# Optimization experiments

Measured on AMD Instinct MI355X. Metric: run time of the kernel, lower is better.

Reference implementation:

```python
import jax, jax.numpy as jnp
import numpy as np

D = 1024
KERNEL = 4

def setup_inputs() -> dict:
    key = jax.random.key(0)
    ks = jax.random.split(key, 8)
    B, L, d = 4, 8192, D
    x = jax.random.normal(ks[0], (B, L, d), dtype=jnp.float32)
    conv_weight = jax.random.normal(ks[1], (d, 1, KERNEL), dtype=jnp.float32) * 0.02
    conv_bias = jnp.zeros((d,), dtype=jnp.float32)
    lim = 1.0 / np.sqrt(d)
    Wr_w = jax.random.uniform(ks[2], (d, d), jnp.float32, -lim, lim)
    Wr_b = jax.random.uniform(ks[3], (d,), jnp.float32, -lim, lim)
    Wi_w = jax.random.uniform(ks[4], (d, d), jnp.float32, -lim, lim)
    Wi_b = jax.random.uniform(ks[5], (d,), jnp.float32, -lim, lim)
    log_a = jnp.full((d,), 7.5, dtype=jnp.float32)
    out_w = jax.random.uniform(ks[6], (d, d), jnp.float32, -lim, lim)
    norm_w = jnp.ones((d,), dtype=jnp.float32)
    return {"x": x, "conv_weight": conv_weight, "conv_bias": conv_bias,
            "Wr_w": Wr_w, "Wr_b": Wr_b, "Wi_w": Wi_w, "Wi_b": Wi_b,
            "log_a": log_a, "out_w": out_w, "norm_w": norm_w}

def _causal_depthwise_conv(x, w, b):
    # x: [B,L,d], w: [d,1,K], b: [d]. out[t] = sum_k w[:,0,k] * x[t-3+k] + b
    B, L, d = x.shape
    xp = jnp.pad(x, ((0, 0), (KERNEL - 1, 0), (0, 0)))
    out = b[None, None, :]
    for k in range(KERNEL):  # small fixed kernel loop
        out = out + xp[:, k:k + L, :] * w[:, 0, k][None, None, :]
    return out

def _parallel_scan(a_t, b_t):
    # h_t = a_t * h_{t-1} + b_t via log-space cumsum; float32 throughout
    a = a_t.astype(jnp.float32)
    b = b_t.astype(jnp.float32)
    log_A = jnp.clip(jnp.cumsum(jnp.log(jnp.clip(a, 1e-7)), axis=1), -80.0, None)
    A = jnp.exp(log_A)
    h = A * jnp.cumsum(b * jnp.exp(-log_A), axis=1)
    return h.astype(a_t.dtype)

def _rmsnorm(x, w, eps=1e-6):
    ms = jnp.mean(jnp.square(x.astype(jnp.float32)), axis=-1, keepdims=True)
    return (x * jax.lax.rsqrt(ms + eps)).astype(x.dtype) * w

def reference(x, conv_weight, conv_bias, Wr_w, Wr_b, Wi_w, Wi_b, log_a, out_w, norm_w):
    x_conv = _causal_depthwise_conv(x, conv_weight, conv_bias)          # [B,L,d]
    r_t = jax.nn.sigmoid(x_conv @ Wr_w.T + Wr_b)
    i_t = jax.nn.sigmoid(x_conv @ Wi_w.T + Wi_b)
    a_base = jax.nn.sigmoid(log_a.astype(jnp.float32)).astype(x.dtype)
    a_t = jnp.power(a_base[None, None, :], 8.0 * r_t)
    b_t = jnp.sqrt(jnp.clip(1.0 - a_t * a_t, 1e-6, None)) * (i_t * x_conv)
    h = _parallel_scan(a_t, b_t)
    return _rmsnorm(h @ out_w.T, norm_w)
```

## Files before the change

### kernel.cpp

```cpp
#include <hip/hip_runtime.h>
#include <hip/hip_bf16.h>

#define D 1024
#define KW 4
#define SEQL 8192
#define BATCH 4
#define MROWS (BATCH*SEQL)
#define SEG 32
#define NSEG (SEQL/SEG)

using bf16 = __hip_bfloat16;
typedef __attribute__((ext_vector_type(8))) short bf16x8_t;
typedef __attribute__((ext_vector_type(4))) float f32x4_t;

__device__ __forceinline__ float sigmoid_f(float x){ return 1.0f/(1.0f + __expf(-x)); }

__device__ __forceinline__ void gload_lds16(const bf16* g, bf16* l){
  __builtin_amdgcn_global_load_lds(
    (const __attribute__((address_space(1))) unsigned int*)g,
    (__attribute__((address_space(3))) unsigned int*)l,
    16, 0, 0);
}

__device__ __forceinline__ void bf16x2_unpack(unsigned int u, float& lo, float& hi){
  union { unsigned int i; float f; } a, b;
  a.i = (u & 0xffffu) << 16;
  b.i = u & 0xffff0000u;
  lo = a.f; hi = b.f;
}
__device__ __forceinline__ unsigned int bf16x2_pack(float lo, float hi){
  unsigned short l = __builtin_bit_cast(unsigned short, __float2bfloat16(lo));
  unsigned short h = __builtin_bit_cast(unsigned short, __float2bfloat16(hi));
  return (unsigned int)l | ((unsigned int)h << 16);
}

__global__ __launch_bounds__(256) void prep_k(const float* __restrict__ Wr, const float* __restrict__ Wi,
                                              const float* __restrict__ Wrb, const float* __restrict__ Wib,
                                              const float* __restrict__ Wo,
                                              bf16* __restrict__ W1, bf16* __restrict__ Wob,
                                              float* __restrict__ b1){
  int idx = blockIdx.x*256 + threadIdx.x;
  if (idx < 2*D*D){
    int n = idx >> 10;
    float v = (n < D) ? Wr[idx] : Wi[idx - D*D];
    W1[idx] = __float2bfloat16(v);
  } else if (idx < 3*D*D){
    int j = idx - 2*D*D;
    Wob[j] = __float2bfloat16(Wo[j]);
  }
  if (idx < 2*D){
    b1[idx] = (idx < D) ? Wrb[idx] : Wib[idx - D];
  }
}

__global__ __launch_bounds__(256) void conv_k(const float* __restrict__ x, const float* __restrict__ w,
                                              const float* __restrict__ bias,
                                              unsigned int* __restrict__ xcb){
  int idx = blockIdx.x*256 + threadIdx.x;
  int c4 = idx & 255;
  int c  = c4 * 4;
  int m  = idx >> 8;
  int l  = m & (SEQL-1);
  const float* wp = w + c*KW;
  f32x4_t t0 = *(const f32x4_t*)(wp);
  f32x4_t t1 = *(const f32x4_t*)(wp + 4);
  f32x4_t t2 = *(const f32x4_t*)(wp + 8);
  f32x4_t t3 = *(const f32x4_t*)(wp + 12);
  f32x4_t bb = *(const f32x4_t*)(bias + c);
  const float* xm = x + (size_t)m*D + c;
  f32x4_t v3 = *(const f32x4_t*)xm;
  f32x4_t z  = (f32x4_t){0.f,0.f,0.f,0.f};
  f32x4_t v2 = (l>=1)? *(const f32x4_t*)(xm - D)   : z;
  f32x4_t v1 = (l>=2)? *(const f32x4_t*)(xm - 2*D) : z;
  f32x4_t v0 = (l>=3)? *(const f32x4_t*)(xm - 3*D) : z;
  float a0 = bb[0] + t0[0]*v0[0] + t0[1]*v1[0] + t0[2]*v2[0] + t0[3]*v3[0];
  float a1 = bb[1] + t1[0]*v0[1] + t1[1]*v1[1] + t1[2]*v2[1] + t1[3]*v3[1];
  float a2 = bb[2] + t2[0]*v0[2] + t2[1]*v1[2] + t2[2]*v2[2] + t2[3]*v3[2];
  float a3 = bb[3] + t3[0]*v0[3] + t3[1]*v1[3] + t3[2]*v2[3] + t3[3]*v3[3];
  uint2 o;
  o.x = bf16x2_pack(a0, a1);
  o.y = bf16x2_pack(a2, a3);
  *(uint2*)(xcb + (size_t)m*512 + 2*c4) = o;
}

template<typename OutT> __device__ __forceinline__ void store_cvt(OutT* p, float v);
template<> __device__ __forceinline__ void store_cvt<float>(float* p, float v){ *p = v; }
template<> __device__ __forceinline__ void store_cvt<bf16>(bf16* p, float v){ *p = __float2bfloat16(v); }

#define MFMA_BF16(a,b,c) __builtin_amdgcn_mfma_f32_16x16x32_bf16((a),(b),(c),0,0,0)

#define GPHASE(buf, q, STAGE_STMT, WAIT_STMT) do{                         \
    bf16x8_t a0 = rdA(buf, 2*(q),   0);                                   \
    bf16x8_t a1 = rdA(buf, 2*(q),   1);                                   \
    bf16x8_t a2 = rdA(buf, 2*(q)+1, 0);                                   \
    bf16x8_t a3 = rdA(buf, 2*(q)+1, 1);                                   \
    if ((q) == 0){                                                        \
      b00 = rdB(buf,0,0); b01 = rdB(buf,0,1);                             \
      b10 = rdB(buf,1,0); b11 = rdB(buf,1,1);                             \
      b20 = rdB(buf,2,0); b21 = rdB(buf,2,1);                             \
      b30 = rdB(buf,3,0); b31 = rdB(buf,3,1);                             \
    }                                                                     \
    STAGE_STMT;                                                           \
    WAIT_STMT;                                                            \
    __builtin_amdgcn_s_barrier();                                         \
    asm volatile("s_waitcnt lgkmcnt(0)" ::: "memory");                    \
    __builtin_amdgcn_s_setprio(1);                                        \
    acc[2*(q)  ][0] = MFMA_BF16(a0, b00, acc[2*(q)  ][0]);                \
    acc[2*(q)  ][0] = MFMA_BF16(a1, b01, acc[2*(q)  ][0]);                \
    acc[2*(q)  ][1] = MFMA_BF16(a0, b10, acc[2*(q)  ][1]);                \
    acc[2*(q)  ][1] = MFMA_BF16(a1, b11, acc[2*(q)  ][1]);                \
    acc[2*(q)  ][2] = MFMA_BF16(a0, b20, acc[2*(q)  ][2]);                \
    acc[2*(q)  ][2] = MFMA_BF16(a1, b21, acc[2*(q)  ][2]);                \
    acc[2*(q)  ][3] = MFMA_BF16(a0, b30, acc[2*(q)  ][3]);                \
    acc[2*(q)  ][3] = MFMA_BF16(a1, b31, acc[2*(q)  ][3]);                \
    acc[2*(q)+1][0] = MFMA_BF16(a2, b00, acc[2*(q)+1][0]);                \
    acc[2*(q)+1][0] = MFMA_BF16(a3, b01, acc[2*(q)+1][0]);                \
    acc[2*(q)+1][1] = MFMA_BF16(a2, b10, acc[2*(q)+1][1]);                \
    acc[2*(q)+1][1] = MFMA_BF16(a3, b11, acc[2*(q)+1][1]);                \
    acc[2*(q)+1][2] = MFMA_BF16(a2, b20, acc[2*(q)+1][2]);                \
    acc[2*(q)+1][2] = MFMA_BF16(a3, b21, acc[2*(q)+1][2]);                \
    acc[2*(q)+1][3] = MFMA_BF16(a2, b30, acc[2*(q)+1][3]);                \
    acc[2*(q)+1][3] = MFMA_BF16(a3, b31, acc[2*(q)+1][3]);                \
    __builtin_amdgcn_s_setprio(0);                                        \
    __builtin_amdgcn_s_barrier();                                         \
}while(0)

#define WAIT_STEADY do{ if (it + 1 < nIter) asm volatile("s_waitcnt vmcnt(4)" ::: "memory"); \
                        else                asm volatile("s_waitcnt vmcnt(0)" ::: "memory"); }while(0)

template<typename OutT, bool HB>
__global__ __launch_bounds__(512, 2) void gemm256(const bf16* __restrict__ A, const bf16* __restrict__ B,
                                                  const float* __restrict__ bias, OutT* __restrict__ C,
                                                  int M, int N, int K){
  __shared__ alignas(128) bf16 Asm[2][256*64];
  __shared__ alignas(128) bf16 Bsm[2][256*64];
  const int t    = threadIdx.x;
  const int wave = t >> 6, lane = t & 63;
  const int wm   = wave >> 2, wn = wave & 3;
  const int lrow = lane & 15, quad = lane >> 4;

  const int nbn = N >> 8;
  const int cpx = gridDim.x >> 3;
  const int bid = blockIdx.x;
  const int swz = (bid & 7) * cpx + (bid >> 3);
  const int m0  = (swz / nbn) << 8;
  const int n0  = (swz % nbn) << 8;

  const int srow = wave*8 + (lane >> 3);
  const int scol = (((lane & 7) ^ (srow & 7)) << 3);

  auto stageA = [&](int tile, int half, int buf){
    const bf16* g = A + (size_t)(m0 + half*128 + srow)*K + tile*64 + scol;
    bf16* l = &Asm[buf][half*128*64 + wave*8*64];
    gload_lds16(g, l);
    gload_lds16(g + (size_t)64*K, l + 64*64);
  };
  auto stageB = [&](int tile, int half, int buf){
    const bf16* g = B + (size_t)(n0 + half*128 + srow)*K + tile*64 + scol;
    bf16* l = &Bsm[buf][half*128*64 + wave*8*64];
    gload_lds16(g, l);
    gload_lds16(g + (size_t)64*K, l + 64*64);
  };
  auto rdA = [&](int buf, int fi, int ks)->bf16x8_t{
    return *(const bf16x8_t*)&Asm[buf][(wm*128 + fi*16 + lrow)*64 + ((((ks)*4 + quad) ^ (lrow & 7)) << 3)];
  };
  auto rdB = [&](int buf, int j, int ks)->bf16x8_t{
    return *(const bf16x8_t*)&Bsm[buf][(wn*64 + j*16 + lrow)*64 + ((((ks)*4 + quad) ^ (lrow & 7)) << 3)];
  };

  f32x4_t acc[8][4];
  #pragma unroll
  for (int i=0;i<8;i++)
    #pragma unroll
    for (int j=0;j<4;j++) acc[i][j] = (f32x4_t){0.f,0.f,0.f,0.f};
  bf16x8_t b00,b01,b10,b11,b20,b21,b30,b31;

  const int nt    = K >> 6;
  const int nIter = nt >> 1;

  stageB(0, 0, 0); stageB(0, 1, 0);
  stageA(0, 0, 0); stageA(0, 1, 0);
  stageB(1, 0, 1); stageB(1, 1, 1);
  asm volatile("s_waitcnt vmcnt(4)" ::: "memory");
  __builtin_amdgcn_s_barrier();

  for (int it = 0; it < nIter; ++it){
    const int t1 = 2*it + 1, t2 = 2*it + 2, t3 = 2*it + 3;
    const bool ok2 = (t2 < nt), ok3 = (t3 < nt);
    GPHASE(0, 0, stageA(t1, 0, 1), );
    GPHASE(0, 1, stageA(t1, 1, 1), );
    GPHASE(0, 2, if (ok2) stageB(t2, 0, 0), );
    GPHASE(0, 3, if (ok2) stageB(t2, 1, 0), WAIT_STEADY);
    GPHASE(1, 0, if (ok2) stageA(t2, 0, 0), );
    GPHASE(1, 1, if (ok2) stageA(t2, 1, 0), );
    GPHASE(1, 2, if (ok3) stageB(t3, 0, 1), );
    GPHASE(1, 3, if (ok3) stageB(t3, 1, 1), WAIT_STEADY);
  }

  #pragma unroll
  for (int i=0;i<8;i++){
    #pragma unroll
    for (int j=0;j<4;j++){
      int gm0 = m0 + wm*128 + i*16 + quad*4;
      int gn  = n0 + wn*64  + j*16 + lrow;
      float bv = HB ? bias[gn] : 0.f;
      #pragma unroll
      for (int r=0;r<4;r++){
        store_cvt(&C[(size_t)(gm0 + r)*N + gn], acc[i][j][r] + bv);
      }
    }
  }
}

__global__ __launch_bounds__(256) void scan1_k(const unsigned int* __restrict__ ri,
                                               const unsigned int* __restrict__ xcb,
                                               const float* __restrict__ log_a,
                                               float* __restrict__ Aprod, float* __restrict__ Hend){
  int idx = blockIdx.x*256 + threadIdx.x;
  int c4 = idx & 255;
  int c  = c4*4;
  int bs = idx >> 8;
  int s  = bs & (NSEG-1);
  int b  = bs >> 8;
  size_t m0 = (size_t)b*SEQL + (size_t)s*SEG;
  f32x4_t la = *(const f32x4_t*)(log_a + c);
  float c1[4];
  #pragma unroll
  for (int j=0;j<4;j++) c1[j] = -8.f * log1pf(__expf(-la[j]));
  float A[4] = {1.f,1.f,1.f,1.f};
  float h[4] = {0.f,0.f,0.f,0.f};
  #pragma unroll 4
  for (int l=0; l<SEG; l++){
    size_t m = m0 + l;
    uint2 uzr = *(const uint2*)(ri  + m*1024 + 2*c4);
    uint2 uzi = *(const uint2*)(ri  + m*1024 + 512 + 2*c4);
    uint2 uxv = *(const uint2*)(xcb + m*512  + 2*c4);
    float zr[4], zi[4], xv[4];
    bf16x2_unpack(uzr.x, zr[0], zr[1]); bf16x2_unpack(uzr.y, zr[2], zr[3]);
    bf16x2_unpack(uzi.x, zi[0], zi[1]); bf16x2_unpack(uzi.y, zi[2], zi[3]);
    bf16x2_unpack(uxv.x, xv[0], xv[1]); bf16x2_unpack(uxv.y, xv[2], xv[3]);
    #pragma unroll
    for (int j=0;j<4;j++){
      float a  = __expf(c1[j] * sigmoid_f(zr[j]));
      float bt = sqrtf(fmaxf(1.f - a*a, 1e-6f)) * sigmoid_f(zi[j]) * xv[j];
      A[j] *= a;
      h[j]  = fmaf(a, h[j], bt);
    }
  }
  *(f32x4_t*)(Aprod + 4*(size_t)idx) = (f32x4_t){A[0],A[1],A[2],A[3]};
  *(f32x4_t*)(Hend  + 4*(size_t)idx) = (f32x4_t){h[0],h[1],h[2],h[3]};
}

__global__ __launch_bounds__(256) void scan2_k(const float* __restrict__ Aprod, const float* __restrict__ Hend,
                                               float* __restrict__ carry){
  int idx = blockIdx.x*256 + threadIdx.x;
  int c = idx & (D-1);
  int b = idx >> 10;
  float h = 0.f;
  #pragma unroll 8
  for (int s=0; s<NSEG; s++){
    int j = ((b*NSEG + s) << 10) + c;
    float a = Aprod[j];
    float e = Hend[j];
    carry[j] = h;
    h = fmaf(a, h, e);
  }
}

__global__ __launch_bounds__(256) void scan3_k(const unsigned int* __restrict__ ri,
                                               unsigned int* xcb,
                                               const float* __restrict__ log_a, const float* __restrict__ carry){
  int idx = blockIdx.x*256 + threadIdx.x;
  int c4 = idx & 255;
  int c  = c4*4;
  int bs = idx >> 8;
  int s  = bs & (NSEG-1);
  int b  = bs >> 8;
  size_t m0 = (size_t)b*SEQL + (size_t)s*SEG;
  f32x4_t la = *(const f32x4_t*)(log_a + c);
  float c1[4];
  #pragma unroll
  for (int j=0;j<4;j++) c1[j] = -8.f * log1pf(__expf(-la[j]));
  f32x4_t h4 = *(const f32x4_t*)(carry + 4*(size_t)idx);
  float h[4] = {h4[0], h4[1], h4[2], h4[3]};
  #pragma unroll 4
  for (int l=0; l<SEG; l++){
    size_t m = m0 + l;
    uint2 uzr = *(const uint2*)(ri  + m*1024 + 2*c4);
    uint2 uzi = *(const uint2*)(ri  + m*1024 + 512 + 2*c4);
    uint2 uxv = *(const uint2*)(xcb + m*512  + 2*c4);
    float zr[4], zi[4], xv[4];
    bf16x2_unpack(uzr.x, zr[0], zr[1]); bf16x2_unpack(uzr.y, zr[2], zr[3]);
    bf16x2_unpack(uzi.x, zi[0], zi[1]); bf16x2_unpack(uzi.y, zi[2], zi[3]);
    bf16x2_unpack(uxv.x, xv[0], xv[1]); bf16x2_unpack(uxv.y, xv[2], xv[3]);
    #pragma unroll
    for (int j=0;j<4;j++){
      float a  = __expf(c1[j] * sigmoid_f(zr[j]));
      float bt = sqrtf(fmaxf(1.f - a*a, 1e-6f)) * sigmoid_f(zi[j]) * xv[j];
      h[j] = fmaf(a, h[j], bt);
    }
    uint2 o;
    o.x = bf16x2_pack(h[0], h[1]);
    o.y = bf16x2_pack(h[2], h[3]);
    *(uint2*)(xcb + m*512 + 2*c4) = o;
  }
}

__global__ __launch_bounds__(256) void rms_k(float* __restrict__ y, const float* __restrict__ nw){
  int row = blockIdx.x;
  int t   = threadIdx.x;
  float* yr = y + (size_t)row*D;
  f32x4_t v = *(const f32x4_t*)(yr + t*4);
  float ss = v[0]*v[0] + v[1]*v[1] + v[2]*v[2] + v[3]*v[3];
  #pragma unroll
  for (int off=32; off>0; off>>=1) ss += __shfl_down(ss, off);
  __shared__ float red[4];
  if ((t & 63) == 0) red[t>>6] = ss;
  __syncthreads();
  float tot = red[0] + red[1] + red[2] + red[3];
  float scale = rsqrtf(tot * (1.f/D) + 1e-6f);
  f32x4_t w = *(const f32x4_t*)(nw + t*4);
  f32x4_t o;
  #pragma unroll
  for (int k=0;k<4;k++) o[k] = v[k]*scale*w[k];
  *(f32x4_t*)(yr + t*4) = o;
}

extern "C" void kernel_launch(void* const* d_in, const int* in_sizes, int n_in,
                              void* d_out, int out_size, void* d_ws, size_t ws_size,
                              hipStream_t stream) {
  const float* x     = (const float*)d_in[0];
  const float* convw = (const float*)d_in[1];
  const float* convb = (const float*)d_in[2];
  const float* Wr_w  = (const float*)d_in[3];
  const float* Wr_b  = (const float*)d_in[4];
  const float* Wi_w  = (const float*)d_in[5];
  const float* Wi_b  = (const float*)d_in[6];
  const float* log_a = (const float*)d_in[7];
  const float* out_w = (const float*)d_in[8];
  const float* norm_w= (const float*)d_in[9];

  char* ws = (char*)d_ws;
  size_t off = 0;
  auto alloc = [&](size_t bytes)->char*{ char* p = ws + off; off += (bytes + 255) & ~(size_t)255; return p; };

  bf16*  xcb   = (bf16*) alloc((size_t)MROWS*D*2);
  bf16*  ri    = (bf16*) alloc((size_t)MROWS*2*D*2);
  bf16*  W1    = (bf16*) alloc((size_t)2*D*D*2);
  bf16*  Wob   = (bf16*) alloc((size_t)D*D*2);
  float* b1    = (float*)alloc((size_t)2*D*4);
  float* Aprod = (float*)alloc((size_t)BATCH*NSEG*D*4);
  float* Hend  = (float*)alloc((size_t)BATCH*NSEG*D*4);
  float* carry = (float*)alloc((size_t)BATCH*NSEG*D*4);
  float* y     = (float*)d_out;

  prep_k<<<dim3((3*D*D + 255)/256), dim3(256), 0, stream>>>(Wr_w, Wi_w, Wr_b, Wi_b, out_w, W1, Wob, b1);
  conv_k<<<dim3(MROWS*(D/4)/256), dim3(256), 0, stream>>>(x, convw, convb, (unsigned int*)xcb);
  gemm256<bf16, true><<<dim3((MROWS/256)*((2*D)/256)), dim3(512), 0, stream>>>(xcb, W1, b1, ri, MROWS, 2*D, D);
  scan1_k<<<dim3(BATCH*NSEG*(D/4)/256), dim3(256), 0, stream>>>((const unsigned int*)ri, (const unsigned int*)xcb, log_a, Aprod, Hend);
  scan2_k<<<dim3(BATCH*D/256), dim3(256), 0, stream>>>(Aprod, Hend, carry);
  scan3_k<<<dim3(BATCH*NSEG*(D/4)/256), dim3(256), 0, stream>>>((const unsigned int*)ri, (unsigned int*)xcb, log_a, carry);
  gemm256<float, false><<<dim3((MROWS/256)*(D/256)), dim3(512), 0, stream>>>(xcb, Wob, nullptr, y, MROWS, D, D);
  rms_k<<<dim3(MROWS), dim3(256), 0, stream>>>(y, norm_w);
}
```

Measured before the change: 696.1 us.

## Stage GEMM epilogue through LDS, parallelize carry scan, batch conv rows and RMSNorm

Several independent changes. The GEMM epilogue now writes accumulators into an LDS tile and then emits coalesced 16-byte row stores instead of scattered per-element stores. The serial scan2 carry pass becomes a wave-level parallel scan over a transposed segment layout, and conv_k computes two rows per thread so overlapping input rows are reused. rms_k processes one row per wave with no LDS reduction or block barrier. The risks are extra barriers in the epilogue, reuse of the A staging buffer as scratch, and strided loads in scan2.

```diff
diff --git a/kernel.cpp b/kernel.cpp
--- a/kernel.cpp
+++ b/kernel.cpp
@@ -8,6 +8,7 @@
 #define MROWS (BATCH*SEQL)
 #define SEG 32
 #define NSEG (SEQL/SEG)
+#define NCHAIN (BATCH*D)
 
 using bf16 = __hip_bfloat16;
 typedef __attribute__((ext_vector_type(8))) short bf16x8_t;
@@ -59,7 +60,8 @@
   int idx = blockIdx.x*256 + threadIdx.x;
   int c4 = idx & 255;
   int c  = c4 * 4;
-  int m  = idx >> 8;
+  int mm = idx >> 8;
+  int m  = mm * 2;
   int l  = m & (SEQL-1);
   const float* wp = w + c*KW;
   f32x4_t t0 = *(const f32x4_t*)(wp);
@@ -68,19 +70,25 @@
   f32x4_t t3 = *(const f32x4_t*)(wp + 12);
   f32x4_t bb = *(const f32x4_t*)(bias + c);
   const float* xm = x + (size_t)m*D + c;
-  f32x4_t v3 = *(const f32x4_t*)xm;
   f32x4_t z  = (f32x4_t){0.f,0.f,0.f,0.f};
-  f32x4_t v2 = (l>=1)? *(const f32x4_t*)(xm - D)   : z;
-  f32x4_t v1 = (l>=2)? *(const f32x4_t*)(xm - 2*D) : z;
-  f32x4_t v0 = (l>=3)? *(const f32x4_t*)(xm - 3*D) : z;
-  float a0 = bb[0] + t0[0]*v0[0] + t0[1]*v1[0] + t0[2]*v2[0] + t0[3]*v3[0];
-  float a1 = bb[1] + t1[0]*v0[1] + t1[1]*v1[1] + t1[2]*v2[1] + t1[3]*v3[1];
-  float a2 = bb[2] + t2[0]*v0[2] + t2[1]*v1[2] + t2[2]*v2[2] + t2[3]*v3[2];
-  float a3 = bb[3] + t3[0]*v0[3] + t3[1]*v1[3] + t3[2]*v2[3] + t3[3]*v3[3];
-  uint2 o;
-  o.x = bf16x2_pack(a0, a1);
-  o.y = bf16x2_pack(a2, a3);
-  *(uint2*)(xcb + (size_t)m*512 + 2*c4) = o;
+  f32x4_t r4 = *(const f32x4_t*)(xm + D);
+  f32x4_t r3 = *(const f32x4_t*)(xm);
+  f32x4_t r2 = (l>=1)? *(const f32x4_t*)(xm - D)   : z;
+  f32x4_t r1 = (l>=2)? *(const f32x4_t*)(xm - 2*D) : z;
+  f32x4_t r0 = (l>=3)? *(const f32x4_t*)(xm - 3*D) : z;
+  float a0 = bb[0] + t0[0]*r0[0] + t0[1]*r1[0] + t0[2]*r2[0] + t0[3]*r3[0];
+  float a1 = bb[1] + t1[0]*r0[1] + t1[1]*r1[1] + t1[2]*r2[1] + t1[3]*r3[1];
+  float a2 = bb[2] + t2[0]*r0[2] + t2[1]*r1[2] + t2[2]*r2[2] + t2[3]*r3[2];
+  float a3 = bb[3] + t3[0]*r0[3] + t3[1]*r1[3] + t3[2]*r2[3] + t3[3]*r3[3];
+  float b0 = bb[0] + t0[0]*r1[0] + t0[1]*r2[0] + t0[2]*r3[0] + t0[3]*r4[0];
+  float b1v= bb[1] + t1[0]*r1[1] + t1[1]*r2[1] + t1[2]*r3[1] + t1[3]*r4[1];
+  float b2 = bb[2] + t2[0]*r1[2] + t2[1]*r2[2] + t2[2]*r3[2] + t2[3]*r4[2];
+  float b3 = bb[3] + t3[0]*r1[3] + t3[1]*r2[3] + t3[2]*r3[3] + t3[3]*r4[3];
+  uint2 o0, o1;
+  o0.x = bf16x2_pack(a0, a1); o0.y = bf16x2_pack(a2, a3);
+  o1.x = bf16x2_pack(b0, b1v); o1.y = bf16x2_pack(b2, b3);
+  *(uint2*)(xcb + (size_t)m*512 + 2*c4)       = o0;
+  *(uint2*)(xcb + (size_t)(m+1)*512 + 2*c4)   = o1;
 }
 
 template<typename OutT> __device__ __forceinline__ void store_cvt(OutT* p, float v);
@@ -197,25 +205,36 @@
     GPHASE(1, 3, if (ok3) stageB(t3, 1, 1), WAIT_STEADY);
   }
 
+  OutT* tile = (OutT*)&Asm[0][0];
+  const int trow = t >> 4;
+  const int tcol = (t & 15) * 16;
+  float bvj[4];
+  #pragma unroll
+  for (int j=0;j<4;j++) bvj[j] = HB ? bias[n0 + wn*64 + j*16 + lrow] : 0.f;
+  const int grow = m0 + (trow >> 4)*128 + (trow & 15);
+
   #pragma unroll
   for (int i=0;i<8;i++){
+    __builtin_amdgcn_s_barrier();
     #pragma unroll
     for (int j=0;j<4;j++){
-      int gm0 = m0 + wm*128 + i*16 + quad*4;
-      int gn  = n0 + wn*64  + j*16 + lrow;
-      float bv = HB ? bias[gn] : 0.f;
+      int lcol = wn*64 + j*16 + lrow;
       #pragma unroll
-      for (int r=0;r<4;r++){
-        store_cvt(&C[(size_t)(gm0 + r)*N + gn], acc[i][j][r] + bv);
-      }
+      for (int r=0;r<4;r++)
+        store_cvt(&tile[(wm*16 + quad*4 + r)*256 + lcol], acc[i][j][r] + bvj[j]);
     }
+    __builtin_amdgcn_s_barrier();
+    const int4* lp = (const int4*)&tile[trow*256 + tcol];
+    int4* gp = (int4*)&C[(size_t)(grow + i*16)*N + n0 + tcol];
+    #pragma unroll
+    for (int q=0; q<(int)sizeof(OutT); ++q) gp[q] = lp[q];
   }
 }
 
 __global__ __launch_bounds__(256) void scan1_k(const unsigned int* __restrict__ ri,
                                                const unsigned int* __restrict__ xcb,
                                                const float* __restrict__ log_a,
-                                               float* __restrict__ Aprod, float* __restrict__ Hend){
+                                               float* __restrict__ AprodT, float* __restrict__ HendT){
   int idx = blockIdx.x*256 + threadIdx.x;
   int c4 = idx & 255;
   int c  = c4*4;
@@ -247,29 +266,45 @@
       h[j]  = fmaf(a, h[j], bt);
     }
   }
-  *(f32x4_t*)(Aprod + 4*(size_t)idx) = (f32x4_t){A[0],A[1],A[2],A[3]};
-  *(f32x4_t*)(Hend  + 4*(size_t)idx) = (f32x4_t){h[0],h[1],h[2],h[3]};
-}
-
-__global__ __launch_bounds__(256) void scan2_k(const float* __restrict__ Aprod, const float* __restrict__ Hend,
-                                               float* __restrict__ carry){
-  int idx = blockIdx.x*256 + threadIdx.x;
-  int c = idx & (D-1);
-  int b = idx >> 10;
-  float h = 0.f;
-  #pragma unroll 8
-  for (int s=0; s<NSEG; s++){
-    int j = ((b*NSEG + s) << 10) + c;
-    float a = Aprod[j];
-    float e = Hend[j];
-    carry[j] = h;
-    h = fmaf(a, h, e);
+  size_t tbase = (size_t)s*NCHAIN + (size_t)b*D + c;
+  *(f32x4_t*)(AprodT + tbase) = (f32x4_t){A[0],A[1],A[2],A[3]};
+  *(f32x4_t*)(HendT  + tbase) = (f32x4_t){h[0],h[1],h[2],h[3]};
+}
+
+__global__ __launch_bounds__(256) void scan2_k(const float* __restrict__ AprodT, const float* __restrict__ HendT,
+                                               float* __restrict__ carryT){
+  int gid   = blockIdx.x*256 + threadIdx.x;
+  int chain = gid >> 6;
+  int lane  = gid & 63;
+  int s0    = lane*4;
+  float a[4], e[4];
+  #pragma unroll
+  for (int k=0;k<4;k++){
+    a[k] = AprodT[(size_t)(s0+k)*NCHAIN + chain];
+    e[k] = HendT [(size_t)(s0+k)*NCHAIN + chain];
+  }
+  float A = a[0], H = e[0];
+  #pragma unroll
+  for (int k=1;k<4;k++){ H = fmaf(a[k], H, e[k]); A *= a[k]; }
+  #pragma unroll
+  for (int off=1; off<64; off<<=1){
+    float Ao = __shfl_up(A, off, 64);
+    float Ho = __shfl_up(H, off, 64);
+    if (lane >= off){ H = fmaf(A, Ho, H); A = A*Ao; }
+  }
+  float Hx = __shfl_up(H, 1, 64);
+  if (lane == 0) Hx = 0.f;
+  float h = Hx;
+  #pragma unroll
+  for (int k=0;k<4;k++){
+    carryT[(size_t)(s0+k)*NCHAIN + chain] = h;
+    h = fmaf(a[k], h, e[k]);
   }
 }
 
 __global__ __launch_bounds__(256) void scan3_k(const unsigned int* __restrict__ ri,
                                                unsigned int* xcb,
-                                               const float* __restrict__ log_a, const float* __restrict__ carry){
+                                               const float* __restrict__ log_a, const float* __restrict__ carryT){
   int idx = blockIdx.x*256 + threadIdx.x;
   int c4 = idx & 255;
   int c  = c4*4;
@@ -281,7 +316,7 @@
   float c1[4];
   #pragma unroll
   for (int j=0;j<4;j++) c1[j] = -8.f * log1pf(__expf(-la[j]));
-  f32x4_t h4 = *(const f32x4_t*)(carry + 4*(size_t)idx);
+  f32x4_t h4 = *(const f32x4_t*)(carryT + (size_t)s*NCHAIN + (size_t)b*D + c);
   float h[4] = {h4[0], h4[1], h4[2], h4[3]};
   #pragma unroll 4
   for (int l=0; l<SEG; l++){
@@ -307,23 +342,26 @@
 }
 
 __global__ __launch_bounds__(256) void rms_k(float* __restrict__ y, const float* __restrict__ nw){
-  int row = blockIdx.x;
-  int t   = threadIdx.x;
-  float* yr = y + (size_t)row*D;
-  f32x4_t v = *(const f32x4_t*)(yr + t*4);
-  float ss = v[0]*v[0] + v[1]*v[1] + v[2]*v[2] + v[3]*v[3];
-  #pragma unroll
-  for (int off=32; off>0; off>>=1) ss += __shfl_down(ss, off);
-  __shared__ float red[4];
-  if ((t & 63) == 0) red[t>>6] = ss;
-  __syncthreads();
-  float tot = red[0] + red[1] + red[2] + red[3];
-  float scale = rsqrtf(tot * (1.f/D) + 1e-6f);
-  f32x4_t w = *(const f32x4_t*)(nw + t*4);
-  f32x4_t o;
-  #pragma unroll
-  for (int k=0;k<4;k++) o[k] = v[k]*scale*w[k];
-  *(f32x4_t*)(yr + t*4) = o;
+  int wave = threadIdx.x >> 6, lane = threadIdx.x & 63;
+  size_t row = (size_t)blockIdx.x*4 + wave;
+  float* yr = y + row*D;
+  f32x4_t v[4];
+  #pragma unroll
+  for (int q=0;q<4;q++) v[q] = *(const f32x4_t*)(yr + q*256 + lane*4);
+  float ss = 0.f;
+  #pragma unroll
+  for (int q=0;q<4;q++) ss += v[q][0]*v[q][0] + v[q][1]*v[q][1] + v[q][2]*v[q][2] + v[q][3]*v[q][3];
+  #pragma unroll
+  for (int off=32; off>0; off>>=1) ss += __shfl_xor(ss, off, 64);
+  float scale = rsqrtf(ss * (1.f/D) + 1e-6f);
+  #pragma unroll
+  for (int q=0;q<4;q++){
+    f32x4_t w = *(const f32x4_t*)(nw + q*256 + lane*4);
+    f32x4_t o;
+    #pragma unroll
+    for (int k=0;k<4;k++) o[k] = v[q][k]*scale*w[k];
+    *(f32x4_t*)(yr + q*256 + lane*4) = o;
+  }
 }
 
 extern "C" void kernel_launch(void* const* d_in, const int* in_sizes, int n_in,
@@ -349,17 +387,17 @@
   bf16*  W1    = (bf16*) alloc((size_t)2*D*D*2);
   bf16*  Wob   = (bf16*) alloc((size_t)D*D*2);
   float* b1    = (float*)alloc((size_t)2*D*4);
-  float* Aprod = (float*)alloc((size_t)BATCH*NSEG*D*4);
-  float* Hend  = (float*)alloc((size_t)BATCH*NSEG*D*4);
-  float* carry = (float*)alloc((size_t)BATCH*NSEG*D*4);
+  float* AprodT= (float*)alloc((size_t)NSEG*NCHAIN*4);
+  float* HendT = (float*)alloc((size_t)NSEG*NCHAIN*4);
+  float* carryT= (float*)alloc((size_t)NSEG*NCHAIN*4);
   float* y     = (float*)d_out;
 
   prep_k<<<dim3((3*D*D + 255)/256), dim3(256), 0, stream>>>(Wr_w, Wi_w, Wr_b, Wi_b, out_w, W1, Wob, b1);
-  conv_k<<<dim3(MROWS*(D/4)/256), dim3(256), 0, stream>>>(x, convw, convb, (unsigned int*)xcb);
+  conv_k<<<dim3((MROWS/2)*(D/4)/256), dim3(256), 0, stream>>>(x, convw, convb, (unsigned int*)xcb);
   gemm256<bf16, true><<<dim3((MROWS/256)*((2*D)/256)), dim3(512), 0, stream>>>(xcb, W1, b1, ri, MROWS, 2*D, D);
-  scan1_k<<<dim3(BATCH*NSEG*(D/4)/256), dim3(256), 0, stream>>>((const unsigned int*)ri, (const unsigned int*)xcb, log_a, Aprod, Hend);
-  scan2_k<<<dim3(BATCH*D/256), dim3(256), 0, stream>>>(Aprod, Hend, carry);
-  scan3_k<<<dim3(BATCH*NSEG*(D/4)/256), dim3(256), 0, stream>>>((const unsigned int*)ri, (unsigned int*)xcb, log_a, carry);
+  scan1_k<<<dim3(BATCH*NSEG*(D/4)/256), dim3(256), 0, stream>>>((const unsigned int*)ri, (const unsigned int*)xcb, log_a, AprodT, HendT);
+  scan2_k<<<dim3(NCHAIN*64/256), dim3(256), 0, stream>>>(AprodT, HendT, carryT);
+  scan3_k<<<dim3(BATCH*NSEG*(D/4)/256), dim3(256), 0, stream>>>((const unsigned int*)ri, (unsigned int*)xcb, log_a, carryT);
   gemm256<float, false><<<dim3((MROWS/256)*(D/256)), dim3(512), 0, stream>>>(xcb, Wob, nullptr, y, MROWS, D, D);
-  rms_k<<<dim3(MROWS), dim3(256), 0, stream>>>(y, norm_w);
-}
+  rms_k<<<dim3(MROWS/4), dim3(256), 0, stream>>>(y, norm_w);
+}
```

Measured after the change: 676.6 us. -2.8%, faster.
